# Optimization experiments

Hardware: AMD Instinct MI355X
Metric: run time of the kernel (lower is better)

## Reference

```python
import math
import jax, jax.numpy as jnp
import numpy as np

D = 192      # d_model
NH = 8       # heads
NL = 2       # levels
NP = 4       # points
HD = D // NH # head dim = 24
GROUPS = 32


def layer_norm(x, g, b, eps=1e-5):
    mu = x.mean(-1, keepdims=True)
    var = ((x - mu) ** 2).mean(-1, keepdims=True)
    return (x - mu) / jnp.sqrt(var + eps) * g + b


def group_norm(x, g, b, eps=1e-5):
    # x: [B, C, H, W]
    B, C, H, W = x.shape
    xg = x.reshape(B, GROUPS, C // GROUPS, H, W)
    mu = xg.mean((2, 3, 4), keepdims=True)
    var = ((xg - mu) ** 2).mean((2, 3, 4), keepdims=True)
    xn = ((xg - mu) / jnp.sqrt(var + eps)).reshape(B, C, H, W)
    return xn * g[None, :, None, None] + b[None, :, None, None]


def pos_embed_2d(H, W):
    # PositionalEncoding2D(96, normalize=True) with an all-valid mask
    eps = 1e-6
    scale = 2 * math.pi
    npf = 96
    y = (jnp.arange(1, H + 1, dtype=jnp.float32) - 0.5) / (H + eps) * scale
    x = (jnp.arange(1, W + 1, dtype=jnp.float32) - 0.5) / (W + eps) * scale
    dim_t = 10000.0 ** (2.0 * (jnp.arange(npf) // 2).astype(jnp.float32) / npf)
    def enc(v):
        p = v[:, None] / dim_t  # [N, 96]
        return jnp.stack([jnp.sin(p[:, 0::2]), jnp.cos(p[:, 1::2])], -1).reshape(v.shape[0], npf)
    pe_y, pe_x = enc(y), enc(x)
    pos = jnp.concatenate([
        jnp.broadcast_to(pe_y[:, None, :], (H, W, npf)),
        jnp.broadcast_to(pe_x[None, :, :], (H, W, npf)),
    ], -1)  # [H, W, 192] (y-part first, like torch cat((pos_y, pos_x)))
    return pos.reshape(H * W, 2 * npf)


def ms_sample(value_h, loc, H, W):
    # value_h: [B, NH, H*W, HD]; loc: [B, NH, Lq, NP, 2] normalized to [0,1]
    # Replicates F.grid_sample(mode='bilinear', padding_mode='zeros', align_corners=False)
    B, _, Lq, P, _ = loc.shape
    x = loc[..., 0] * W - 0.5
    y = loc[..., 1] * H - 0.5
    x0 = jnp.floor(x)
    y0 = jnp.floor(y)
    wx = x - x0
    wy = y - y0
    def corner(xc, yc, w):
        valid = (xc >= 0) & (xc <= W - 1) & (yc >= 0) & (yc <= H - 1)
        xi = jnp.clip(xc, 0, W - 1).astype(jnp.int32)
        yi = jnp.clip(yc, 0, H - 1).astype(jnp.int32)
        idx = (yi * W + xi).reshape(B, NH, Lq * P)
        g = jnp.take_along_axis(value_h, idx[..., None], axis=2).reshape(B, NH, Lq, P, HD)
        return g * (w * valid)[..., None]
    return (corner(x0, y0, (1 - wx) * (1 - wy))
            + corner(x0 + 1, y0, wx * (1 - wy))
            + corner(x0, y0 + 1, (1 - wx) * wy)
            + corner(x0 + 1, y0 + 1, wx * wy))


def encoder_forward(src, pos, ref_pts, shapes, p):
    B, L, _ = src.shape
    starts = np.cumsum([0] + [h * w for h, w in shapes])
    offset_norm = jnp.array([[w, h] for h, w in shapes], jnp.float32)  # [NL, 2] = (W, H)
    out = src
    n_layers = p['so_W'].shape[0]
    for i in range(n_layers):
        q = out + pos
        off = (q @ p['so_W'][i] + p['so_b'][i]).reshape(B, L, NH, NL, NP, 2)
        aw = (q @ p['aw_W'][i] + p['aw_b'][i]).reshape(B, L, NH, NL * NP)
        aw = jax.nn.softmax(aw, -1).reshape(B, L, NH, NL, NP)
        loc = ref_pts[None, :, None, :, None, :] + off / offset_norm[None, None, None, :, None, :]
        v = (out @ p['vp_W'][i] + p['vp_b'][i]).reshape(B, L, NH, HD).transpose(0, 2, 1, 3)
        sampled = []
        for l, (h, w) in enumerate(shapes):
            vl = v[:, :, starts[l]:starts[l + 1], :]
            locl = loc[:, :, :, l].transpose(0, 2, 1, 3, 4)  # [B, NH, L, NP, 2]
            sampled.append(ms_sample(vl, locl, h, w))
        sampled = jnp.stack(sampled, 3)  # [B, NH, L, NL, NP, HD]
        awh = aw.transpose(0, 2, 1, 3, 4)  # [B, NH, L, NL, NP]
        attn = jnp.einsum('bhqlp,bhqlpc->bhqc', awh, sampled)
        attn = attn.transpose(0, 2, 1, 3).reshape(B, L, D)
        attn = attn @ p['op_W'][i] + p['op_b'][i]
        out = layer_norm(out + attn, p['ln1_g'][i], p['ln1_b'][i])
        ff = jax.nn.relu(out @ p['l1_W'][i] + p['l1_b'][i]) @ p['l2_W'][i] + p['l2_b'][i]
        out = layer_norm(out + ff, p['ln2_g'][i], p['ln2_b'][i])
    return out


def _feature_encoder(feat0, feat1, proj_w0, proj_b0, gn_g0, gn_b0,
                     proj_w1, proj_b1, gn_g1, gn_b1, level_embed, p):
    feats = [feat0, feat1]
    projs = [(proj_w0, proj_b0, gn_g0, gn_b0), (proj_w1, proj_b1, gn_g1, gn_b1)]
    shapes = [(int(f.shape[2]), int(f.shape[3])) for f in feats]
    B = feat0.shape[0]
    srcs, poss, refs = [], [], []
    for l, f in enumerate(feats):
        w, b, g, bb = projs[l]
        s = jnp.einsum('bchw,oc->bohw', f, w) + b[None, :, None, None]  # 1x1 conv
        s = group_norm(s, g, bb)
        srcs.append(s.reshape(B, D, -1).transpose(0, 2, 1))
        poss.append(pos_embed_2d(*shapes[l]) + level_embed[l])
        h, wdt = shapes[l]
        ry, rx = jnp.meshgrid(jnp.linspace(0.5, h - 0.5, h) / h,
                              jnp.linspace(0.5, wdt - 0.5, wdt) / wdt, indexing='ij')
        refs.append(jnp.stack([rx.reshape(-1), ry.reshape(-1)], -1))
    src = jnp.concatenate(srcs, 1)                # [B, Ltot, D]
    pos = jnp.concatenate(poss, 0)[None]          # [1, Ltot, D]
    # full-size images => masks all False => valid_ratios == 1
    ref_pts = jnp.broadcast_to(jnp.concatenate(refs, 0)[:, None, :], (src.shape[1], NL, 2))
    mem = encoder_forward(src, pos, ref_pts, shapes, p)
    n0 = shapes[0][0] * shapes[0][1]
    m0 = mem[:, :n0].reshape(B, shapes[0][0], shapes[0][1], D).transpose(0, 3, 1, 2)
    m1 = mem[:, n0:].reshape(B, shapes[1][0], shapes[1][1], D).transpose(0, 3, 1, 2)
    return m0, m1


def setup_inputs() -> dict:
    key = jax.random.key(0)
    ks = jax.random.split(key, 20)
    L = 6
    s = 0.02
    d = {}
    d['feat0'] = jax.random.normal(ks[0], (2, D, 96, 96), jnp.float32)
    d['feat1'] = jax.random.normal(ks[1], (2, D, 48, 48), jnp.float32)
    d['imgs'] = jax.random.normal(ks[2], (2, 3, 384, 384), jnp.float32)
    d['proj_w0'] = jax.random.normal(ks[3], (D, D), jnp.float32) * s
    d['proj_b0'] = jnp.zeros((D,), jnp.float32)
    d['gn_g0'] = jnp.ones((D,), jnp.float32)
    d['gn_b0'] = jnp.zeros((D,), jnp.float32)
    d['proj_w1'] = jax.random.normal(ks[4], (D, D), jnp.float32) * s
    d['proj_b1'] = jnp.zeros((D,), jnp.float32)
    d['gn_g1'] = jnp.ones((D,), jnp.float32)
    d['gn_b1'] = jnp.zeros((D,), jnp.float32)
    d['level_embed'] = jax.random.normal(ks[5], (NL, D), jnp.float32) * s
    d['so_W'] = jax.random.normal(ks[6], (L, D, NH * NL * NP * 2), jnp.float32) * s
    d['so_b'] = jax.random.normal(ks[7], (L, NH * NL * NP * 2), jnp.float32) * s
    d['aw_W'] = jax.random.normal(ks[8], (L, D, NH * NL * NP), jnp.float32) * s
    d['aw_b'] = jnp.zeros((L, NH * NL * NP), jnp.float32)
    d['vp_W'] = jax.random.normal(ks[9], (L, D, D), jnp.float32) * s
    d['vp_b'] = jnp.zeros((L, D), jnp.float32)
    d['op_W'] = jax.random.normal(ks[10], (L, D, D), jnp.float32) * s
    d['op_b'] = jnp.zeros((L, D), jnp.float32)
    d['ln1_g'] = jnp.ones((L, D), jnp.float32)
    d['ln1_b'] = jnp.zeros((L, D), jnp.float32)
    d['l1_W'] = jax.random.normal(ks[11], (L, D, 256), jnp.float32) * s
    d['l1_b'] = jnp.zeros((L, 256), jnp.float32)
    d['l2_W'] = jax.random.normal(ks[12], (L, 256, D), jnp.float32) * s
    d['l2_b'] = jnp.zeros((L, D), jnp.float32)
    d['ln2_g'] = jnp.ones((L, D), jnp.float32)
    d['ln2_b'] = jnp.zeros((L, D), jnp.float32)
    return d


def reference(feat0, feat1, imgs, proj_w0, proj_b0, gn_g0, gn_b0,
              proj_w1, proj_b1, gn_g1, gn_b1, level_embed,
              so_W, so_b, aw_W, aw_b, vp_W, vp_b, op_W, op_b,
              ln1_g, ln1_b, l1_W, l1_b, l2_W, l2_b, ln2_g, ln2_b):
    # imgs is only used for image sizes; full-size => all-valid masks
    p = dict(so_W=so_W, so_b=so_b, aw_W=aw_W, aw_b=aw_b, vp_W=vp_W, vp_b=vp_b,
             op_W=op_W, op_b=op_b, ln1_g=ln1_g, ln1_b=ln1_b,
             l1_W=l1_W, l1_b=l1_b, l2_W=l2_W, l2_b=l2_b, ln2_g=ln2_g, ln2_b=ln2_b)
    return _feature_encoder(feat0, feat1, proj_w0, proj_b0, gn_g0, gn_b0,
                            proj_w1, proj_b1, gn_g1, gn_b1, level_embed, p)
```

## Files before the change

### kernel.cpp

```cpp
#include <hip/hip_runtime.h>
#include <hip/hip_bf16.h>
#include <math.h>

#define Bb 2
#define Dm 192
#define NHh 8
#define HDd 24
#define N0 9216
#define N1 2304
#define LSEQ 11520
#define FFD 256
#define Mrows (Bb*LSEQ)

typedef __attribute__((ext_vector_type(8))) short short8;
typedef __attribute__((ext_vector_type(4))) float f32x4;

#define F_OUT 0
#define F_PRE (F_OUT + 4423680)
#define F_POS (F_PRE + 4423680)
#define F_LOC (F_POS + 2211840)
#define F_AW  (F_LOC + 2949120)
#define F_QB  (F_AW + 1474560)
#define F_OB  (F_QB + 2211840)
#define F_AH  (F_OB + 2211840)
#define F_WT16 (F_AH + 2949120)
#define F_BC  (F_WT16 + 626688)
#define F_GNS (F_BC + 1152)

#define WL_STRIDE 208896
#define WL_SOAW 0
#define WL_VP   36864
#define WL_OP   73728
#define WL_L1   110592
#define WL_L2   159744

__device__ inline __hip_bfloat16 f2b(float f) { return __float2bfloat16(f); }
__device__ inline unsigned short f2bu(float f) {
    __hip_bfloat16 h = __float2bfloat16(f);
    return *reinterpret_cast<unsigned short*>(&h);
}

__global__ void k_pos(float* pos, const float* level_embed) {
    int idx = blockIdx.x * 256 + threadIdx.x;
    if (idx >= LSEQ * Dm) return;
    int t = idx / Dm, d = idx % Dm;
    int lvl, row, col, H, W;
    if (t < N0) { lvl = 0; H = 96; W = 96; row = t / 96; col = t % 96; }
    else        { lvl = 1; H = 48; W = 48; int tl = t - N0; row = tl / 48; col = tl % 48; }
    int k = d % 96;
    float v;
    if (d < 96) v = (row + 0.5f) / ((float)H + 1e-6f) * 6.2831853071795864f;
    else        v = (col + 0.5f) / ((float)W + 1e-6f) * 6.2831853071795864f;
    float expo = (float)(k - (k & 1)) / 96.0f;
    float tm = exp2f(expo * 13.287712379549449f);
    float p = v / tm;
    float pe = (k & 1) ? cosf(p) : sinf(p);
    pos[idx] = pe + level_embed[lvl * Dm + d];
}

__global__ void k_prep(const float* soW, const float* awW, const float* vpW,
        const float* opW, const float* l1W, const float* l2W,
        const float* sob, const float* awb,
        __hip_bfloat16* WT, float* BC) {
    int idx = blockIdx.x * 256 + threadIdx.x;
    if (idx < 6 * 192) {
        int i = idx / 192, n = idx % 192;
        BC[idx] = (n < 128) ? sob[i * 128 + n] : awb[i * 64 + (n - 128)];
    }
    if (idx >= 6 * WL_STRIDE) return;
    int i = idx / WL_STRIDE; int r = idx % WL_STRIDE;
    float v;
    if (r < 36864)       { int n = r / 192, k = r % 192;
        v = (n < 128) ? soW[((size_t)i * 192 + k) * 128 + n]
                      : awW[((size_t)i * 192 + k) * 64 + (n - 128)]; }
    else if (r < 73728)  { int q = r - 36864;  int n = q / 192, k = q % 192;
        v = vpW[((size_t)i * 192 + k) * 192 + n]; }
    else if (r < 110592) { int q = r - 73728;  int n = q / 192, k = q % 192;
        v = opW[((size_t)i * 192 + k) * 192 + n]; }
    else if (r < 159744) { int q = r - 110592; int n = q / 192, k = q % 192;
        v = l1W[((size_t)i * 192 + k) * 256 + n]; }
    else                 { int q = r - 159744; int n = q / 256, k = q % 256;
        v = l2W[((size_t)i * 256 + k) * 192 + n]; }
    WT[idx] = f2b(v);
}

__global__ void k_prepc(const float* w0, const float* w1, __hip_bfloat16* cwb) {
    int idx = blockIdx.x * 256 + threadIdx.x;
    if (idx >= 2 * 36864) return;
    const float* w = (idx < 36864) ? w0 : w1;
    int r = idx % 36864;
    cwb[idx] = f2b(w[r]);
}

__global__ void k_tf(const float* feat, __hip_bfloat16* out, int HW, int st) {
    __shared__ float tile[32][33];
    int t0 = blockIdx.x * 32, c0 = blockIdx.y * 32, b = blockIdx.z;
    int tx = threadIdx.x, ty = threadIdx.y;
    #pragma unroll
    for (int k = 0; k < 4; k++) {
        int c = c0 + ty + k * 8;
        tile[ty + k * 8][tx] = feat[((size_t)b * Dm + c) * HW + t0 + tx];
    }
    __syncthreads();
    #pragma unroll
    for (int k = 0; k < 4; k++) {
        int t = t0 + ty + k * 8;
        out[((size_t)b * LSEQ + st + t) * Dm + c0 + tx] = f2b(tile[tx][ty + k * 8]);
    }
}

__global__ __launch_bounds__(192) void k_gnp(const float* __restrict__ pre,
        float* __restrict__ part) {
    int bid = blockIdx.x;
    int b = bid / 120; int r = bid % 120;
    int l = (r >= 96) ? 1 : 0; int ch = l ? (r - 96) : r;
    int start = b * LSEQ + (l ? N0 : 0) + ch * 96;
    int d = threadIdx.x;
    float s = 0.f, sq = 0.f;
    for (int t = 0; t < 96; t++) {
        float x = pre[(size_t)(start + t) * Dm + d];
        s += x; sq += x * x;
    }
    __shared__ float ls[192], lq[192];
    ls[d] = s; lq[d] = sq;
    __syncthreads();
    if (d < 32) {
        float a = 0.f, b2 = 0.f;
        #pragma unroll
        for (int j = 0; j < 6; j++) { a += ls[d * 6 + j]; b2 += lq[d * 6 + j]; }
        part[((size_t)bid * 32 + d) * 2]     = a;
        part[((size_t)bid * 32 + d) * 2 + 1] = b2;
    }
}

__global__ void k_gnf(const float* __restrict__ part, float* __restrict__ gns) {
    int bid = blockIdx.x;
    int b = bid >> 6; int l = (bid >> 5) & 1; int g = bid & 31;
    int nch = l ? 24 : 96;
    int base = b * 120 + (l ? 96 : 0);
    int tid = threadIdx.x;
    float s = 0.f, q = 0.f;
    for (int c = tid; c < nch; c += 64) {
        s += part[((size_t)(base + c) * 32 + g) * 2];
        q += part[((size_t)(base + c) * 32 + g) * 2 + 1];
    }
    for (int m = 1; m < 64; m <<= 1) { s += __shfl_xor(s, m, 64); q += __shfl_xor(q, m, 64); }
    if (tid == 0) {
        float total = (float)((l ? N1 : N0) * 6);
        float mean = s / total;
        float var = q / total - mean * mean;
        gns[bid * 2] = mean;
        gns[bid * 2 + 1] = rsqrtf(var + 1e-5f);
    }
}

__global__ void k_gnnorm(const float* srcp, const float* gns,
        const float* g0, const float* b0, const float* g1, const float* b1,
        const float* pos, float* out, __hip_bfloat16* ob, __hip_bfloat16* qb) {
    int idx = blockIdx.x * 256 + threadIdx.x;
    if (idx >= Bb * LSEQ * Dm) return;
    int d = idx % Dm;
    int t = (idx / Dm) % LSEQ;
    int l = (t < N0) ? 0 : 1;
    int g = d / 6;
    int b = idx / (Dm * LSEQ);
    int sid = ((b * 2 + l) * 32 + g) * 2;
    float mean = gns[sid], rstd = gns[sid + 1];
    float gg = l ? g1[d] : g0[d];
    float bbv = l ? b1[d] : b0[d];
    float v = (srcp[idx] - mean) * rstd * gg + bbv;
    out[idx] = v;
    ob[idx] = f2b(v);
    qb[idx] = f2b(v + pos[idx - (size_t)b * LSEQ * Dm]);
}

template<int KSTEPS>
__global__ __launch_bounds__(256) void k_gemm(
        const __hip_bfloat16* __restrict__ A,
        const __hip_bfloat16* __restrict__ Bt,
        const float* __restrict__ bias,
        float* __restrict__ Cf, int N) {
    constexpr int K = KSTEPS * 32;
    int wid = threadIdx.x >> 6, lane = threadIdx.x & 63;
    int lg = lane >> 4, lr = lane & 15;
    int row0 = blockIdx.x * 64 + wid * 16;
    int col0 = blockIdx.y * 64;
    const short* a_base = (const short*)A + (size_t)(row0 + lr) * K + lg * 8;
    const short* b_base = (const short*)Bt + (size_t)(col0 + lr) * K + lg * 8;
    f32x4 acc[4] = {};
    #pragma unroll
    for (int kk = 0; kk < KSTEPS; kk++) {
        short8 af = *(const short8*)(a_base + kk * 32);
        #pragma unroll
        for (int n = 0; n < 4; n++) {
            short8 bfr = *(const short8*)(b_base + (size_t)n * 16 * K + kk * 32);
            acc[n] = __builtin_amdgcn_mfma_f32_16x16x32_bf16(af, bfr, acc[n], 0, 0, 0);
        }
    }
    #pragma unroll
    for (int n = 0; n < 4; n++) {
        int col = col0 + n * 16 + lr;
        float bv = bias[col];
        #pragma unroll
        for (int r = 0; r < 4; r++) {
            int row = row0 + lg * 4 + r;
            Cf[(size_t)row * N + col] = acc[n][r] + bv;
        }
    }
}

__global__ __launch_bounds__(192) void k_soawvp(
        const __hip_bfloat16* __restrict__ QB,
        const __hip_bfloat16* __restrict__ OB,
        const __hip_bfloat16* __restrict__ BtS,
        const __hip_bfloat16* __restrict__ BtV,
        const float* __restrict__ biasS,
        const float* __restrict__ biasV,
        float* __restrict__ LOC, float* __restrict__ AW,
        float* __restrict__ VF) {
    constexpr int K = 192;
    int wid = threadIdx.x >> 6, lane = threadIdx.x & 63;
    int lg = lane >> 4, lr = lane & 15;
    int row0 = blockIdx.x * 32;
    int col0 = wid * 64;
    int role = blockIdx.y;
    const short* A  = (const short*)(role ? OB : QB);
    const short* Bt = (const short*)(role ? BtV : BtS);
    const float* bias = role ? biasV : biasS;
    short8 bw[24];
    {
        const short* b_base = Bt + (size_t)(col0 + lr) * K + lg * 8;
        #pragma unroll
        for (int n = 0; n < 4; n++)
            #pragma unroll
            for (int kk = 0; kk < 6; kk++)
                bw[n * 6 + kk] = *(const short8*)(b_base + (size_t)n * 16 * K + kk * 32);
    }
    #pragma unroll
    for (int rg = 0; rg < 2; rg++) {
        const short* a_base = A + (size_t)(row0 + rg * 16 + lr) * K + lg * 8;
        f32x4 acc[4] = {};
        #pragma unroll
        for (int kk = 0; kk < 6; kk++) {
            short8 af = *(const short8*)(a_base + kk * 32);
            #pragma unroll
            for (int n = 0; n < 4; n++)
                acc[n] = __builtin_amdgcn_mfma_f32_16x16x32_bf16(af, bw[n * 6 + kk], acc[n], 0, 0, 0);
        }
        #pragma unroll
        for (int n = 0; n < 4; n++) {
            float bv = bias[col0 + n * 16 + lr];
            #pragma unroll
            for (int r = 0; r < 4; r++) acc[n][r] += bv;
        }
        int rbase = row0 + rg * 16;
        if (role) {
            #pragma unroll
            for (int n = 0; n < 4; n++) {
                int col = col0 + n * 16 + lr;
                #pragma unroll
                for (int r = 0; r < 4; r++)
                    VF[(size_t)(rbase + lg * 4 + r) * Dm + col] = acc[n][r];
            }
        } else if (wid == 2) {
            #pragma unroll
            for (int n = 0; n < 4; n++) {
                #pragma unroll
                for (int r = 0; r < 4; r++) {
                    float v = acc[n][r];
                    float m = v;
                    m = fmaxf(m, __shfl_xor(m, 1)); m = fmaxf(m, __shfl_xor(m, 2));
                    m = fmaxf(m, __shfl_xor(m, 4));
                    float e = expf(v - m);
                    float sm = e;
                    sm += __shfl_xor(sm, 1); sm += __shfl_xor(sm, 2); sm += __shfl_xor(sm, 4);
                    AW[(size_t)(rbase + lg * 4 + r) * 64 + n * 16 + lr] = e / sm;
                }
            }
        } else {
            #pragma unroll
            for (int r = 0; r < 4; r++) {
                int row = rbase + lg * 4 + r;
                int t = (row >= LSEQ) ? row - LSEQ : row;
                int rr, cc, Ht, Wt;
                if (t < N0) { Ht = 96; Wt = 96; rr = t / 96; cc = t % 96; }
                else        { Ht = 48; Wt = 48; int tl = t - N0; rr = tl / 48; cc = tl % 48; }
                float refx = (cc + 0.5f) / (float)Wt;
                float refy = (rr + 0.5f) / (float)Ht;
                #pragma unroll
                for (int n = 0; n < 4; n++) {
                    int col = col0 + n * 16 + lr;
                    int j = col >> 1, comp = col & 1;
                    float sc = (j & 4) ? 48.f : 96.f;
                    LOC[(size_t)row * 128 + col] = (comp ? refy : refx) + acc[n][r] / sc;
                }
            }
        }
    }
}

__global__ __launch_bounds__(256) void k_tail(
        const __hip_bfloat16* __restrict__ ATT,
        const __hip_bfloat16* __restrict__ BtOp, const float* __restrict__ bOp,
        const __hip_bfloat16* __restrict__ Bt1, const float* __restrict__ b1,
        const __hip_bfloat16* __restrict__ Bt2, const float* __restrict__ b2,
        const float* __restrict__ g1, const float* __restrict__ t1,
        const float* __restrict__ g2, const float* __restrict__ t2,
        const float* __restrict__ pos,
        float* __restrict__ OUTp, __hip_bfloat16* __restrict__ ob,
        __hip_bfloat16* __restrict__ qb) {
    __shared__ __align__(16) short ybf[32][200];
    __shared__ __align__(16) short hid[32][264];
    __shared__ float ps[4][32], pq[4][32];
    int tid = threadIdx.x;
    int wid = tid >> 6, lane = tid & 63, lg = lane >> 4, lr = lane & 15;
    int row0 = blockIdx.x * 32;
    float yres[2][3][4];
    {
        float resid[2][3][4];
        #pragma unroll
        for (int rg = 0; rg < 2; rg++)
            #pragma unroll
            for (int n = 0; n < 3; n++) {
                int col = wid * 48 + n * 16 + lr;
                #pragma unroll
                for (int r = 0; r < 4; r++)
                    resid[rg][n][r] = OUTp[(size_t)(row0 + rg * 16 + lg * 4 + r) * Dm + col];
            }
        const short* a0 = (const short*)ATT + (size_t)(row0 + lr) * 192 + lg * 8;
        const short* a1 = (const short*)ATT + (size_t)(row0 + 16 + lr) * 192 + lg * 8;
        const short* b_base = (const short*)BtOp + (size_t)(wid * 48 + lr) * 192 + lg * 8;
        f32x4 acc[2][3] = {};
        #pragma unroll
        for (int kk = 0; kk < 6; kk++) {
            short8 af0 = *(const short8*)(a0 + kk * 32);
            short8 af1 = *(const short8*)(a1 + kk * 32);
            #pragma unroll
            for (int n = 0; n < 3; n++) {
                short8 bfr = *(const short8*)(b_base + (size_t)n * 16 * 192 + kk * 32);
                acc[0][n] = __builtin_amdgcn_mfma_f32_16x16x32_bf16(af0, bfr, acc[0][n], 0, 0, 0);
                acc[1][n] = __builtin_amdgcn_mfma_f32_16x16x32_bf16(af1, bfr, acc[1][n], 0, 0, 0);
            }
        }
        #pragma unroll
        for (int rg = 0; rg < 2; rg++) {
            float s[4] = {0.f, 0.f, 0.f, 0.f}, q[4] = {0.f, 0.f, 0.f, 0.f};
            #pragma unroll
            for (int n = 0; n < 3; n++) {
                int col = wid * 48 + n * 16 + lr;
                float bv = bOp[col];
                #pragma unroll
                for (int r = 0; r < 4; r++) {
                    float v = acc[rg][n][r] + bv + resid[rg][n][r];
                    acc[rg][n][r] = v;
                    s[r] += v; q[r] += v * v;
                }
            }
            #pragma unroll
            for (int r = 0; r < 4; r++) {
                #pragma unroll
                for (int m = 1; m < 16; m <<= 1) {
                    s[r] += __shfl_xor(s[r], m); q[r] += __shfl_xor(q[r], m);
                }
            }
            if (lr == 0) {
                #pragma unroll
                for (int r = 0; r < 4; r++) {
                    ps[wid][rg * 16 + lg * 4 + r] = s[r];
                    pq[wid][rg * 16 + lg * 4 + r] = q[r];
                }
            }
        }
        __syncthreads();
        #pragma unroll
        for (int rg = 0; rg < 2; rg++) {
            float mean[4], rstd[4];
            #pragma unroll
            for (int r = 0; r < 4; r++) {
                int rl = rg * 16 + lg * 4 + r;
                float S = ps[0][rl] + ps[1][rl] + ps[2][rl] + ps[3][rl];
                float Q = pq[0][rl] + pq[1][rl] + pq[2][rl] + pq[3][rl];
                mean[r] = S * (1.f / Dm);
                float var = Q * (1.f / Dm) - mean[r] * mean[r];
                rstd[r] = rsqrtf(var + 1e-5f);
            }
            #pragma unroll
            for (int n = 0; n < 3; n++) {
                int col = wid * 48 + n * 16 + lr;
                float gg = g1[col], bb = t1[col];
                #pragma unroll
                for (int r = 0; r < 4; r++) {
                    float y = (acc[rg][n][r] - mean[r]) * rstd[r] * gg + bb;
                    yres[rg][n][r] = y;
                    ybf[rg * 16 + lg * 4 + r][col] = (short)f2bu(y);
                }
            }
        }
        __syncthreads();
    }
    {
        const short* b_base = (const short*)Bt1 + (size_t)(wid * 64 + lr) * 192 + lg * 8;
        f32x4 acc[2][4] = {};
        #pragma unroll
        for (int kk = 0; kk < 6; kk++) {
            short8 af0 = *(const short8*)&ybf[lr][lg * 8 + kk * 32];
            short8 af1 = *(const short8*)&ybf[16 + lr][lg * 8 + kk * 32];
            #pragma unroll
            for (int n = 0; n < 4; n++) {
                short8 bfr = *(const short8*)(b_base + (size_t)n * 16 * 192 + kk * 32);
                acc[0][n] = __builtin_amdgcn_mfma_f32_16x16x32_bf16(af0, bfr, acc[0][n], 0, 0, 0);
                acc[1][n] = __builtin_amdgcn_mfma_f32_16x16x32_bf16(af1, bfr, acc[1][n], 0, 0, 0);
            }
        }
        #pragma unroll
        for (int rg = 0; rg < 2; rg++)
            #pragma unroll
            for (int n = 0; n < 4; n++) {
                int col = wid * 64 + n * 16 + lr;
                float bv = b1[col];
                #pragma unroll
                for (int r = 0; r < 4; r++)
                    hid[rg * 16 + lg * 4 + r][col] = (short)f2bu(fmaxf(acc[rg][n][r] + bv, 0.f));
            }
        __syncthreads();
    }
    {
        const short* b_base = (const short*)Bt2 + (size_t)(wid * 48 + lr) * 256 + lg * 8;
        f32x4 acc[2][3] = {};
        #pragma unroll
        for (int kk = 0; kk < 8; kk++) {
            short8 af0 = *(const short8*)&hid[lr][lg * 8 + kk * 32];
            short8 af1 = *(const short8*)&hid[16 + lr][lg * 8 + kk * 32];
            #pragma unroll
            for (int n = 0; n < 3; n++) {
                short8 bfr = *(const short8*)(b_base + (size_t)n * 16 * 256 + kk * 32);
                acc[0][n] = __builtin_amdgcn_mfma_f32_16x16x32_bf16(af0, bfr, acc[0][n], 0, 0, 0);
                acc[1][n] = __builtin_amdgcn_mfma_f32_16x16x32_bf16(af1, bfr, acc[1][n], 0, 0, 0);
            }
        }
        #pragma unroll
        for (int rg = 0; rg < 2; rg++) {
            float s[4] = {0.f, 0.f, 0.f, 0.f}, q[4] = {0.f, 0.f, 0.f, 0.f};
            #pragma unroll
            for (int n = 0; n < 3; n++) {
                int col = wid * 48 + n * 16 + lr;
                float bv = b2[col];
                #pragma unroll
                for (int r = 0; r < 4; r++) {
                    float v = acc[rg][n][r] + bv + yres[rg][n][r];
                    acc[rg][n][r] = v;
                    s[r] += v; q[r] += v * v;
                }
            }
            #pragma unroll
            for (int r = 0; r < 4; r++) {
                #pragma unroll
                for (int m = 1; m < 16; m <<= 1) {
                    s[r] += __shfl_xor(s[r], m); q[r] += __shfl_xor(q[r], m);
                }
            }
            if (lr == 0) {
                #pragma unroll
                for (int r = 0; r < 4; r++) {
                    ps[wid][rg * 16 + lg * 4 + r] = s[r];
                    pq[wid][rg * 16 + lg * 4 + r] = q[r];
                }
            }
        }
        __syncthreads();
        #pragma unroll
        for (int rg = 0; rg < 2; rg++) {
            float mean[4], rstd[4];
            #pragma unroll
            for (int r = 0; r < 4; r++) {
                int rl = rg * 16 + lg * 4 + r;
                float S = ps[0][rl] + ps[1][rl] + ps[2][rl] + ps[3][rl];
                float Q = pq[0][rl] + pq[1][rl] + pq[2][rl] + pq[3][rl];
                mean[r] = S * (1.f / Dm);
                float var = Q * (1.f / Dm) - mean[r] * mean[r];
                rstd[r] = rsqrtf(var + 1e-5f);
            }
            #pragma unroll
            for (int n = 0; n < 3; n++) {
                int col = wid * 48 + n * 16 + lr;
                float gg = g2[col], bb = t2[col];
                #pragma unroll
                for (int r = 0; r < 4; r++) {
                    int row = row0 + rg * 16 + lg * 4 + r;
                    size_t o = (size_t)row * Dm + col;
                    float y = (acc[rg][n][r] - mean[r]) * rstd[r] * gg + bb;
                    OUTp[o] = y;
                    ob[o] = f2b(y);
                    int tp = (row >= LSEQ) ? row - LSEQ : row;
                    qb[o] = f2b(y + pos[(size_t)tp * Dm + col]);
                }
            }
        }
    }
}

__global__ __launch_bounds__(192) void k_sample(const float* __restrict__ V,
        const float* __restrict__ LOC, const float* __restrict__ AW,
        __hip_bfloat16* __restrict__ ATT) {
    __shared__ float aw_s[4][64];
    __shared__ float loc_s[4][128];
    int tid = threadIdx.x;
    int tg0 = blockIdx.x * 4;
    for (int idx = tid; idx < 256; idx += 192)
        aw_s[idx >> 6][idx & 63] = AW[(size_t)tg0 * 64 + idx];
    for (int idx = tid; idx < 512; idx += 192)
        loc_s[idx >> 7][idx & 127] = LOC[(size_t)tg0 * 128 + idx];
    __syncthreads();
    int tt = tid / 48, lane = tid - tt * 48;
    int h = lane / 6, dq = lane - h * 6;
    int tg = tg0 + tt;
    int b = (tg >= LSEQ) ? 1 : 0;
    const float* vb = V + (size_t)b * LSEQ * Dm + h * HDd + dq * 4;
    float a0 = 0.f, a1 = 0.f, a2 = 0.f, a3 = 0.f;
    #pragma unroll
    for (int lp = 0; lp < 8; lp++) {
        int l = lp >> 2;
        int Wl = l ? 48 : 96, Hl = l ? 48 : 96, st = l ? N0 : 0;
        float a  = aw_s[tt][h * 8 + lp];
        float lx = loc_s[tt][(h * 8 + lp) * 2];
        float ly = loc_s[tt][(h * 8 + lp) * 2 + 1];
        float x = lx * (float)Wl - 0.5f, y = ly * (float)Hl - 0.5f;
        float x0f = floorf(x), y0f = floorf(y);
        float wx = x - x0f, wy = y - y0f;
        int x0 = (int)x0f, y0 = (int)y0f;
        #pragma unroll
        for (int cy = 0; cy < 2; cy++) {
            int yi = y0 + cy;
            float wyv = cy ? wy : 1.f - wy;
            bool vy = (yi >= 0) && (yi < Hl);
            int yc = min(max(yi, 0), Hl - 1);
            #pragma unroll
            for (int cx = 0; cx < 2; cx++) {
                int xi = x0 + cx;
                float wv = (cx ? wx : 1.f - wx) * wyv;
                bool ok = vy && (xi >= 0) && (xi < Wl);
                int xc = min(max(xi, 0), Wl - 1);
                float cw = ok ? a * wv : 0.f;
                float4 g4 = *(const float4*)(vb + (size_t)(st + yc * Wl + xc) * Dm);
                a0 += cw * g4.x; a1 += cw * g4.y;
                a2 += cw * g4.z; a3 += cw * g4.w;
            }
        }
    }
    ushort4 o4;
    o4.x = f2bu(a0); o4.y = f2bu(a1); o4.z = f2bu(a2); o4.w = f2bu(a3);
    *(ushort4*)((unsigned short*)ATT + (size_t)tg * Dm + h * HDd + dq * 4) = o4;
}

__global__ void k_outt(const float* __restrict__ out, float* __restrict__ dst,
        int HW, int st) {
    __shared__ float tile[32][33];
    int t0 = blockIdx.x * 32, d0 = blockIdx.y * 32, b = blockIdx.z;
    int tx = threadIdx.x, ty = threadIdx.y;
    #pragma unroll
    for (int k = 0; k < 4; k++) {
        int t = t0 + ty + k * 8;
        tile[ty + k * 8][tx] = out[((size_t)b * LSEQ + st + t) * Dm + d0 + tx];
    }
    __syncthreads();
    #pragma unroll
    for (int k = 0; k < 4; k++) {
        int d = d0 + ty + k * 8;
        dst[((size_t)b * Dm + d) * HW + t0 + tx] = tile[tx][ty + k * 8];
    }
}

extern "C" void kernel_launch(void* const* d_in, const int* in_sizes, int n_in,
                              void* d_out, int out_size, void* d_ws, size_t ws_size,
                              hipStream_t stream) {
    (void)in_sizes; (void)n_in; (void)out_size; (void)ws_size;
    const float* feat0   = (const float*)d_in[0];
    const float* feat1   = (const float*)d_in[1];
    const float* proj_w0 = (const float*)d_in[3];
    const float* proj_b0 = (const float*)d_in[4];
    const float* gn_g0   = (const float*)d_in[5];
    const float* gn_b0   = (const float*)d_in[6];
    const float* proj_w1 = (const float*)d_in[7];
    const float* proj_b1 = (const float*)d_in[8];
    const float* gn_g1   = (const float*)d_in[9];
    const float* gn_b1   = (const float*)d_in[10];
    const float* level_embed = (const float*)d_in[11];
    const float* so_W = (const float*)d_in[12];
    const float* so_b = (const float*)d_in[13];
    const float* aw_W = (const float*)d_in[14];
    const float* aw_b = (const float*)d_in[15];
    const float* vp_W = (const float*)d_in[16];
    const float* vp_b = (const float*)d_in[17];
    const float* op_W = (const float*)d_in[18];
    const float* op_b = (const float*)d_in[19];
    const float* ln1_g = (const float*)d_in[20];
    const float* ln1_b = (const float*)d_in[21];
    const float* l1_W = (const float*)d_in[22];
    const float* l1_b = (const float*)d_in[23];
    const float* l2_W = (const float*)d_in[24];
    const float* l2_b = (const float*)d_in[25];
    const float* ln2_g = (const float*)d_in[26];
    const float* ln2_b = (const float*)d_in[27];

    float* ws   = (float*)d_ws;
    float* OUT  = ws + F_OUT;
    float* PRE  = ws + F_PRE;
    float* POS  = ws + F_POS;
    float* LOC  = ws + F_LOC;
    float* AWp  = ws + F_AW;
    __hip_bfloat16* QB  = (__hip_bfloat16*)(ws + F_QB);
    __hip_bfloat16* OB  = (__hip_bfloat16*)(ws + F_OB);
    __hip_bfloat16* AH  = (__hip_bfloat16*)(ws + F_AH);
    __hip_bfloat16* WT16 = (__hip_bfloat16*)(ws + F_WT16);
    float* BC   = ws + F_BC;
    float* GNS  = ws + F_GNS;
    __hip_bfloat16* FEATB = (__hip_bfloat16*)(ws + F_LOC);
    __hip_bfloat16* CWB   = (__hip_bfloat16*)(ws + F_AW);
    float* GPART = ws + F_AH;

    k_pos<<<(LSEQ * Dm + 255) / 256, 256, 0, stream>>>(POS, level_embed);
    k_prep<<<(6 * WL_STRIDE + 255) / 256, 256, 0, stream>>>(so_W, aw_W, vp_W, op_W,
        l1_W, l2_W, so_b, aw_b, WT16, BC);
    k_prepc<<<(2 * 36864 + 255) / 256, 256, 0, stream>>>(proj_w0, proj_w1, CWB);
    k_tf<<<dim3(N0 / 32, 6, 2), dim3(32, 8), 0, stream>>>(feat0, FEATB, N0, 0);
    k_tf<<<dim3(N1 / 32, 6, 2), dim3(32, 8), 0, stream>>>(feat1, FEATB, N1, N0);
    for (int b = 0; b < 2; b++) {
        k_gemm<6><<<dim3(N0 / 64, 3), 256, 0, stream>>>(
            FEATB + (size_t)b * LSEQ * Dm, CWB, proj_b0,
            PRE + (size_t)b * LSEQ * Dm, Dm);
        k_gemm<6><<<dim3(N1 / 64, 3), 256, 0, stream>>>(
            FEATB + ((size_t)b * LSEQ + N0) * Dm, CWB + 36864, proj_b1,
            PRE + ((size_t)b * LSEQ + N0) * Dm, Dm);
    }
    k_gnp<<<240, 192, 0, stream>>>(PRE, GPART);
    k_gnf<<<128, 64, 0, stream>>>(GPART, GNS);
    k_gnnorm<<<(Bb * LSEQ * Dm + 255) / 256, 256, 0, stream>>>(PRE, GNS,
        gn_g0, gn_b0, gn_g1, gn_b1, POS, OUT, OB, QB);

    for (int i = 0; i < 6; i++) {
        const __hip_bfloat16* WL = WT16 + (size_t)i * WL_STRIDE;
        k_soawvp<<<dim3(Mrows / 32, 2), 192, 0, stream>>>(
            QB, OB, WL + WL_SOAW, WL + WL_VP, BC + i * 192,
            vp_b + (size_t)i * Dm, LOC, AWp, PRE);
        k_sample<<<Mrows / 4, 192, 0, stream>>>(PRE, LOC, AWp, AH);
        k_tail<<<Mrows / 32, 256, 0, stream>>>(
            AH, WL + WL_OP, op_b + (size_t)i * Dm,
            WL + WL_L1, l1_b + (size_t)i * FFD,
            WL + WL_L2, l2_b + (size_t)i * Dm,
            ln1_g + (size_t)i * Dm, ln1_b + (size_t)i * Dm,
            ln2_g + (size_t)i * Dm, ln2_b + (size_t)i * Dm, POS,
            OUT, OB, QB);
    }
    k_outt<<<dim3(N0 / 32, 6, 2), dim3(32, 8), 0, stream>>>(OUT, (float*)d_out, N0, 0);
    k_outt<<<dim3(N1 / 32, 6, 2), dim3(32, 8), 0, stream>>>(OUT,
        (float*)d_out + (size_t)Bb * Dm * N0, N1, N0);
}
```

Before: 619.8 us.

## Fuse deformable sampling and next-layer projections into the tail kernel

Moves the bilinear sampling into the start of k_tail, keeping the sampled features in shared memory instead of a global bf16 buffer. It also appends the next layer's value, offset and attention-weight projections, with softmax, to the end of the same kernel, using the freshly normalised rows kept in LDS. The value tensor is double-buffered across layers because sampling reads arbitrary rows. This removes two kernel launches per layer and the global round-trips for the sampled features and the OB/QB activations. In exchange each block uses more LDS and runs a latency-bound gather phase, which may lower occupancy.

```diff
diff --git a/kernel.cpp b/kernel.cpp
--- a/kernel.cpp
+++ b/kernel.cpp
@@ -26,6 +26,7 @@
 #define F_WT16 (F_AH + 2949120)
 #define F_BC  (F_WT16 + 626688)
 #define F_GNS (F_BC + 1152)
+#define F_V2  (F_GNS + 256)
 
 #define WL_STRIDE 208896
 #define WL_SOAW 0
@@ -299,24 +300,82 @@
     }
 }
 
+template<bool LAST>
 __global__ __launch_bounds__(256) void k_tail(
-        const __hip_bfloat16* __restrict__ ATT,
+        const float* __restrict__ Vin,
+        float* __restrict__ LOC, float* __restrict__ AW,
         const __hip_bfloat16* __restrict__ BtOp, const float* __restrict__ bOp,
         const __hip_bfloat16* __restrict__ Bt1, const float* __restrict__ b1,
         const __hip_bfloat16* __restrict__ Bt2, const float* __restrict__ b2,
         const float* __restrict__ g1, const float* __restrict__ t1,
         const float* __restrict__ g2, const float* __restrict__ t2,
         const float* __restrict__ pos,
-        float* __restrict__ OUTp, __hip_bfloat16* __restrict__ ob,
-        __hip_bfloat16* __restrict__ qb) {
+        float* __restrict__ OUTp,
+        const __hip_bfloat16* __restrict__ BtS,
+        const __hip_bfloat16* __restrict__ BtV,
+        const float* __restrict__ biasS, const float* __restrict__ biasV,
+        float* __restrict__ Vout) {
     __shared__ __align__(16) short ybf[32][200];
     __shared__ __align__(16) short hid[32][264];
+    __shared__ float aw_s[32][64];
     __shared__ float ps[4][32], pq[4][32];
     int tid = threadIdx.x;
     int wid = tid >> 6, lane = tid & 63, lg = lane >> 4, lr = lane & 15;
     int row0 = blockIdx.x * 32;
     float yres[2][3][4];
     {
+        float* loc_s = (float*)&hid[0][0];
+        for (int idx = tid; idx < 32 * 128; idx += 256)
+            loc_s[idx] = LOC[(size_t)row0 * 128 + idx];
+        for (int idx = tid; idx < 32 * 64; idx += 256)
+            aw_s[idx >> 6][idx & 63] = AW[(size_t)row0 * 64 + idx];
+        __syncthreads();
+        for (int tt6 = 0; tt6 < 6; tt6++) {
+            int id = tid + tt6 * 256;
+            int tl = id / 48;
+            int l48 = id - tl * 48;
+            int h = l48 / 6, dq = l48 - h * 6;
+            int row = row0 + tl;
+            int bb = (row >= LSEQ) ? 1 : 0;
+            const float* vbase = Vin + (size_t)bb * LSEQ * Dm + h * HDd + dq * 4;
+            float a0 = 0.f, a1 = 0.f, a2 = 0.f, a3 = 0.f;
+            #pragma unroll
+            for (int lp = 0; lp < 8; lp++) {
+                int l = lp >> 2;
+                int Wl = l ? 48 : 96, Hl = l ? 48 : 96, st = l ? N0 : 0;
+                float a  = aw_s[tl][h * 8 + lp];
+                float lx = loc_s[tl * 128 + (h * 8 + lp) * 2];
+                float ly = loc_s[tl * 128 + (h * 8 + lp) * 2 + 1];
+                float x = lx * (float)Wl - 0.5f, y = ly * (float)Hl - 0.5f;
+                float x0f = floorf(x), y0f = floorf(y);
+                float wx = x - x0f, wy = y - y0f;
+                int x0 = (int)x0f, y0 = (int)y0f;
+                #pragma unroll
+                for (int cy = 0; cy < 2; cy++) {
+                    int yi = y0 + cy;
+                    float wyv = cy ? wy : 1.f - wy;
+                    bool vy = (yi >= 0) && (yi < Hl);
+                    int yc = min(max(yi, 0), Hl - 1);
+                    #pragma unroll
+                    for (int cx = 0; cx < 2; cx++) {
+                        int xi = x0 + cx;
+                        float wv = (cx ? wx : 1.f - wx) * wyv;
+                        bool ok = vy && (xi >= 0) && (xi < Wl);
+                        int xc = min(max(xi, 0), Wl - 1);
+                        float cw = ok ? a * wv : 0.f;
+                        float4 g4 = *(const float4*)(vbase + (size_t)(st + yc * Wl + xc) * Dm);
+                        a0 += cw * g4.x; a1 += cw * g4.y;
+                        a2 += cw * g4.z; a3 += cw * g4.w;
+                    }
+                }
+            }
+            ushort4 o4;
+            o4.x = f2bu(a0); o4.y = f2bu(a1); o4.z = f2bu(a2); o4.w = f2bu(a3);
+            *(ushort4*)&ybf[tl][h * HDd + dq * 4] = o4;
+        }
+        __syncthreads();
+    }
+    {
         float resid[2][3][4];
         #pragma unroll
         for (int rg = 0; rg < 2; rg++)
@@ -327,14 +386,12 @@
                 for (int r = 0; r < 4; r++)
                     resid[rg][n][r] = OUTp[(size_t)(row0 + rg * 16 + lg * 4 + r) * Dm + col];
             }
-        const short* a0 = (const short*)ATT + (size_t)(row0 + lr) * 192 + lg * 8;
-        const short* a1 = (const short*)ATT + (size_t)(row0 + 16 + lr) * 192 + lg * 8;
         const short* b_base = (const short*)BtOp + (size_t)(wid * 48 + lr) * 192 + lg * 8;
         f32x4 acc[2][3] = {};
         #pragma unroll
         for (int kk = 0; kk < 6; kk++) {
-            short8 af0 = *(const short8*)(a0 + kk * 32);
-            short8 af1 = *(const short8*)(a1 + kk * 32);
+            short8 af0 = *(const short8*)&ybf[lr][lg * 8 + kk * 32];
+            short8 af1 = *(const short8*)&ybf[16 + lr][lg * 8 + kk * 32];
             #pragma unroll
             for (int n = 0; n < 3; n++) {
                 short8 bfr = *(const short8*)(b_base + (size_t)n * 16 * 192 + kk * 32);
@@ -487,69 +544,96 @@
                 #pragma unroll
                 for (int r = 0; r < 4; r++) {
                     int row = row0 + rg * 16 + lg * 4 + r;
-                    size_t o = (size_t)row * Dm + col;
+                    int rl = rg * 16 + lg * 4 + r;
                     float y = (acc[rg][n][r] - mean[r]) * rstd[r] * gg + bb;
-                    OUTp[o] = y;
-                    ob[o] = f2b(y);
-                    int tp = (row >= LSEQ) ? row - LSEQ : row;
-                    qb[o] = f2b(y + pos[(size_t)tp * Dm + col]);
-                }
-            }
-        }
-    }
-}
-
-__global__ __launch_bounds__(192) void k_sample(const float* __restrict__ V,
-        const float* __restrict__ LOC, const float* __restrict__ AW,
-        __hip_bfloat16* __restrict__ ATT) {
-    __shared__ float aw_s[4][64];
-    __shared__ float loc_s[4][128];
-    int tid = threadIdx.x;
-    int tg0 = blockIdx.x * 4;
-    for (int idx = tid; idx < 256; idx += 192)
-        aw_s[idx >> 6][idx & 63] = AW[(size_t)tg0 * 64 + idx];
-    for (int idx = tid; idx < 512; idx += 192)
-        loc_s[idx >> 7][idx & 127] = LOC[(size_t)tg0 * 128 + idx];
+                    OUTp[(size_t)row * Dm + col] = y;
+                    if (!LAST) {
+                        ybf[rl][col] = (short)f2bu(y);
+                        int tp = (row >= LSEQ) ? row - LSEQ : row;
+                        hid[rl][col] = (short)f2bu(y + pos[(size_t)tp * Dm + col]);
+                    }
+                }
+            }
+        }
+    }
+    if (LAST) return;
     __syncthreads();
-    int tt = tid / 48, lane = tid - tt * 48;
-    int h = lane / 6, dq = lane - h * 6;
-    int tg = tg0 + tt;
-    int b = (tg >= LSEQ) ? 1 : 0;
-    const float* vb = V + (size_t)b * LSEQ * Dm + h * HDd + dq * 4;
-    float a0 = 0.f, a1 = 0.f, a2 = 0.f, a3 = 0.f;
-    #pragma unroll
-    for (int lp = 0; lp < 8; lp++) {
-        int l = lp >> 2;
-        int Wl = l ? 48 : 96, Hl = l ? 48 : 96, st = l ? N0 : 0;
-        float a  = aw_s[tt][h * 8 + lp];
-        float lx = loc_s[tt][(h * 8 + lp) * 2];
-        float ly = loc_s[tt][(h * 8 + lp) * 2 + 1];
-        float x = lx * (float)Wl - 0.5f, y = ly * (float)Hl - 0.5f;
-        float x0f = floorf(x), y0f = floorf(y);
-        float wx = x - x0f, wy = y - y0f;
-        int x0 = (int)x0f, y0 = (int)y0f;
-        #pragma unroll
-        for (int cy = 0; cy < 2; cy++) {
-            int yi = y0 + cy;
-            float wyv = cy ? wy : 1.f - wy;
-            bool vy = (yi >= 0) && (yi < Hl);
-            int yc = min(max(yi, 0), Hl - 1);
-            #pragma unroll
-            for (int cx = 0; cx < 2; cx++) {
-                int xi = x0 + cx;
-                float wv = (cx ? wx : 1.f - wx) * wyv;
-                bool ok = vy && (xi >= 0) && (xi < Wl);
-                int xc = min(max(xi, 0), Wl - 1);
-                float cw = ok ? a * wv : 0.f;
-                float4 g4 = *(const float4*)(vb + (size_t)(st + yc * Wl + xc) * Dm);
-                a0 += cw * g4.x; a1 += cw * g4.y;
-                a2 += cw * g4.z; a3 += cw * g4.w;
-            }
-        }
-    }
-    ushort4 o4;
-    o4.x = f2bu(a0); o4.y = f2bu(a1); o4.z = f2bu(a2); o4.w = f2bu(a3);
-    *(ushort4*)((unsigned short*)ATT + (size_t)tg * Dm + h * HDd + dq * 4) = o4;
+    {
+        const short* b_base = (const short*)BtV + (size_t)(wid * 48 + lr) * 192 + lg * 8;
+        f32x4 acc[2][3] = {};
+        #pragma unroll
+        for (int kk = 0; kk < 6; kk++) {
+            short8 af0 = *(const short8*)&ybf[lr][lg * 8 + kk * 32];
+            short8 af1 = *(const short8*)&ybf[16 + lr][lg * 8 + kk * 32];
+            #pragma unroll
+            for (int n = 0; n < 3; n++) {
+                short8 bfr = *(const short8*)(b_base + (size_t)n * 16 * 192 + kk * 32);
+                acc[0][n] = __builtin_amdgcn_mfma_f32_16x16x32_bf16(af0, bfr, acc[0][n], 0, 0, 0);
+                acc[1][n] = __builtin_amdgcn_mfma_f32_16x16x32_bf16(af1, bfr, acc[1][n], 0, 0, 0);
+            }
+        }
+        #pragma unroll
+        for (int rg = 0; rg < 2; rg++)
+            #pragma unroll
+            for (int n = 0; n < 3; n++) {
+                int col = wid * 48 + n * 16 + lr;
+                float bv = biasV[col];
+                #pragma unroll
+                for (int r = 0; r < 4; r++)
+                    Vout[(size_t)(row0 + rg * 16 + lg * 4 + r) * Dm + col] = acc[rg][n][r] + bv;
+            }
+    }
+    {
+        const short* b_base = (const short*)BtS + (size_t)(wid * 48 + lr) * 192 + lg * 8;
+        f32x4 acc[2][3] = {};
+        #pragma unroll
+        for (int kk = 0; kk < 6; kk++) {
+            short8 af0 = *(const short8*)&hid[lr][lg * 8 + kk * 32];
+            short8 af1 = *(const short8*)&hid[16 + lr][lg * 8 + kk * 32];
+            #pragma unroll
+            for (int n = 0; n < 3; n++) {
+                short8 bfr = *(const short8*)(b_base + (size_t)n * 16 * 192 + kk * 32);
+                acc[0][n] = __builtin_amdgcn_mfma_f32_16x16x32_bf16(af0, bfr, acc[0][n], 0, 0, 0);
+                acc[1][n] = __builtin_amdgcn_mfma_f32_16x16x32_bf16(af1, bfr, acc[1][n], 0, 0, 0);
+            }
+        }
+        #pragma unroll
+        for (int rg = 0; rg < 2; rg++) {
+            #pragma unroll
+            for (int n = 0; n < 3; n++) {
+                int col = wid * 48 + n * 16 + lr;
+                float bv = biasS[col];
+                if (col >= 128) {
+                    #pragma unroll
+                    for (int r = 0; r < 4; r++) {
+                        float v = acc[rg][n][r] + bv;
+                        float m = v;
+                        m = fmaxf(m, __shfl_xor(m, 1)); m = fmaxf(m, __shfl_xor(m, 2));
+                        m = fmaxf(m, __shfl_xor(m, 4));
+                        float e = expf(v - m);
+                        float sm = e;
+                        sm += __shfl_xor(sm, 1); sm += __shfl_xor(sm, 2); sm += __shfl_xor(sm, 4);
+                        AW[(size_t)(row0 + rg * 16 + lg * 4 + r) * 64 + (col - 128)] = e / sm;
+                    }
+                } else {
+                    #pragma unroll
+                    for (int r = 0; r < 4; r++) {
+                        int row = row0 + rg * 16 + lg * 4 + r;
+                        int t = (row >= LSEQ) ? row - LSEQ : row;
+                        int rr, cc, Ht, Wt;
+                        if (t < N0) { Ht = 96; Wt = 96; rr = t / 96; cc = t % 96; }
+                        else        { Ht = 48; Wt = 48; int tl = t - N0; rr = tl / 48; cc = tl % 48; }
+                        float refx = (cc + 0.5f) / (float)Wt;
+                        float refy = (rr + 0.5f) / (float)Ht;
+                        int j = col >> 1;
+                        float sc = (j & 4) ? 48.f : 96.f;
+                        LOC[(size_t)row * 128 + col] =
+                            ((col & 1) ? refy : refx) + (acc[rg][n][r] + bv) / sc;
+                    }
+                }
+            }
+        }
+    }
 }
 
 __global__ void k_outt(const float* __restrict__ out, float* __restrict__ dst,
@@ -608,9 +692,9 @@
     float* POS  = ws + F_POS;
     float* LOC  = ws + F_LOC;
     float* AWp  = ws + F_AW;
+    float* V2   = ws + F_V2;
     __hip_bfloat16* QB  = (__hip_bfloat16*)(ws + F_QB);
     __hip_bfloat16* OB  = (__hip_bfloat16*)(ws + F_OB);
-    __hip_bfloat16* AH  = (__hip_bfloat16*)(ws + F_AH);
     __hip_bfloat16* WT16 = (__hip_bfloat16*)(ws + F_WT16);
     float* BC   = ws + F_BC;
     float* GNS  = ws + F_GNS;
@@ -637,19 +721,35 @@
     k_gnnorm<<<(Bb * LSEQ * Dm + 255) / 256, 256, 0, stream>>>(PRE, GNS,
         gn_g0, gn_b0, gn_g1, gn_b1, POS, OUT, OB, QB);
 
+    k_soawvp<<<dim3(Mrows / 32, 2), 192, 0, stream>>>(
+        QB, OB, WT16 + WL_SOAW, WT16 + WL_VP, BC, vp_b, LOC, AWp, V2);
+
+    float* Vin = V2;
+    float* Vout = PRE;
     for (int i = 0; i < 6; i++) {
         const __hip_bfloat16* WL = WT16 + (size_t)i * WL_STRIDE;
-        k_soawvp<<<dim3(Mrows / 32, 2), 192, 0, stream>>>(
-            QB, OB, WL + WL_SOAW, WL + WL_VP, BC + i * 192,
-            vp_b + (size_t)i * Dm, LOC, AWp, PRE);
-        k_sample<<<Mrows / 4, 192, 0, stream>>>(PRE, LOC, AWp, AH);
-        k_tail<<<Mrows / 32, 256, 0, stream>>>(
-            AH, WL + WL_OP, op_b + (size_t)i * Dm,
-            WL + WL_L1, l1_b + (size_t)i * FFD,
-            WL + WL_L2, l2_b + (size_t)i * Dm,
-            ln1_g + (size_t)i * Dm, ln1_b + (size_t)i * Dm,
-            ln2_g + (size_t)i * Dm, ln2_b + (size_t)i * Dm, POS,
-            OUT, OB, QB);
+        if (i < 5) {
+            const __hip_bfloat16* WN = WT16 + (size_t)(i + 1) * WL_STRIDE;
+            k_tail<false><<<Mrows / 32, 256, 0, stream>>>(
+                Vin, LOC, AWp,
+                WL + WL_OP, op_b + (size_t)i * Dm,
+                WL + WL_L1, l1_b + (size_t)i * FFD,
+                WL + WL_L2, l2_b + (size_t)i * Dm,
+                ln1_g + (size_t)i * Dm, ln1_b + (size_t)i * Dm,
+                ln2_g + (size_t)i * Dm, ln2_b + (size_t)i * Dm, POS, OUT,
+                WN + WL_SOAW, WN + WL_VP, BC + (i + 1) * 192,
+                vp_b + (size_t)(i + 1) * Dm, Vout);
+        } else {
+            k_tail<true><<<Mrows / 32, 256, 0, stream>>>(
+                Vin, LOC, AWp,
+                WL + WL_OP, op_b + (size_t)i * Dm,
+                WL + WL_L1, l1_b + (size_t)i * FFD,
+                WL + WL_L2, l2_b + (size_t)i * Dm,
+                ln1_g + (size_t)i * Dm, ln1_b + (size_t)i * Dm,
+                ln2_g + (size_t)i * Dm, ln2_b + (size_t)i * Dm, POS, OUT,
+                nullptr, nullptr, nullptr, nullptr, nullptr);
+        }
+        float* tswap = Vin; Vin = Vout; Vout = tswap;
     }
     k_outt<<<dim3(N0 / 32, 6, 2), dim3(32, 8), 0, stream>>>(OUT, (float*)d_out, N0, 0);
     k_outt<<<dim3(N1 / 32, 6, 2), dim3(32, 8), 0, stream>>>(OUT,
```

Measured after the change: 642.5 us. 1.04x slower.
